# Kernel optimization log

Measured on AMD Instinct MI355X. Metric: run time of the kernel, lower is better.

The kernel has to match this reference:

```python
import jax, jax.numpy as jnp
import numpy as np

N = 50000   # num entities
R2 = 480    # num_rels * 2
D = 200     # h_dim
T = 4       # sequence_len (graph snapshots)
E = 100000  # edges per snapshot
L = 2       # rgcn layers
SLOPE = (1.0 / 8.0 + 1.0 / 3.0) / 2.0  # deterministic rrelu (eval-mode expected slope)


def setup_inputs() -> dict:
    key = jax.random.key(0)
    ks = jax.random.split(key, 13)
    s = 1.0 / np.sqrt(D)
    w = lambda k, shp, sc: jax.random.normal(k, shp, dtype=jnp.float32) * sc
    return {
        "src": jax.random.randint(ks[0], (T, E), 0, N, dtype=jnp.int32),
        "dst": jax.random.randint(ks[1], (T, E), 0, N, dtype=jnp.int32),
        "etype": jax.random.randint(ks[2], (T, E), 0, R2, dtype=jnp.int32),
        "dynamic_emb": w(ks[3], (N, D), 1.0),
        "emb_rel": w(ks[4], (R2, D), s),
        "W_ih": w(ks[5], (3 * D, 2 * D), s),
        "W_hh": w(ks[6], (3 * D, D), s),
        "b_ih": jnp.zeros((3 * D,), jnp.float32),
        "b_hh": jnp.zeros((3 * D,), jnp.float32),
        "W_neighbor": w(ks[7], (L, D, D), s),
        "W_loop": w(ks[8], (L, D, D), s),
        "time_gate_weight": w(ks[9], (D, D), s),
        "time_gate_bias": jnp.zeros((D,), jnp.float32),
    }


def _l2norm(x):
    n = jnp.linalg.norm(x, axis=-1, keepdims=True)
    return x / jnp.maximum(n, 1e-12)


def _gru(x, hprev, W_ih, W_hh, b_ih, b_hh):
    gi = x @ W_ih.T + b_ih
    gh = hprev @ W_hh.T + b_hh
    ir, iz, inn = jnp.split(gi, 3, axis=-1)
    hr, hz, hn = jnp.split(gh, 3, axis=-1)
    r = jax.nn.sigmoid(ir + hr)
    z = jax.nn.sigmoid(iz + hz)
    n = jnp.tanh(inn + r * hn)
    return (1.0 - z) * n + z * hprev


def reference(src, dst, etype, dynamic_emb, emb_rel, W_ih, W_hh, b_ih, b_hh,
              W_neighbor, W_loop, time_gate_weight, time_gate_bias):
    h_init = _l2norm(dynamic_emb)  # layer_norm=True path (F.normalize)

    def step(carry, g):
        h, h0 = carry
        s, d_, et = g
        # per-relation mean of entity embeddings touching that relation (r_to_e spans)
        ent_idx = jnp.concatenate([s, d_])          # [2E]
        seg = jnp.concatenate([et, et])             # [2E]
        ssum = jax.ops.segment_sum(h[ent_idx], seg, num_segments=R2)
        cnt = jax.ops.segment_sum(jnp.ones_like(seg, jnp.float32), seg, num_segments=R2)
        x_mean = ssum / jnp.maximum(cnt, 1.0)[:, None]          # absent rels stay 0
        x_input = jnp.concatenate([emb_rel, x_mean], axis=1)    # [R2, 2D]
        h0 = _l2norm(_gru(x_input, h0, W_ih, W_hh, b_ih, b_hh))
        # UnionRGCNLayer x L: gather -> sum-aggregate -> norm + self-loop -> rrelu
        deg = jax.ops.segment_sum(jnp.ones_like(d_, jnp.float32), d_, num_segments=N)
        norm = 1.0 / jnp.maximum(deg, 1.0)
        hh = h
        for l in range(L):
            pre = hh[s] + h0[et]                                  # [E, D]
            agg = jax.ops.segment_sum(pre, d_, num_segments=N) @ W_neighbor[l]
            out = agg * norm[:, None] + hh @ W_loop[l]
            hh = jnp.where(out >= 0, out, out * SLOPE)            # rrelu (eval)
        cur = _l2norm(hh)
        tw = jax.nn.sigmoid(h @ time_gate_weight + time_gate_bias)
        h = tw * cur + (1.0 - tw) * h
        return (h, h0), h

    (_, _), hist = jax.lax.scan(step, (h_init, emb_rel), (src, dst, etype))
    return hist  # [T, N, D] history of evolved entity embeddings
```

## Files before the change

### kernel.cpp

```cpp
#include <hip/hip_runtime.h>
#include <math.h>

#define NE 50000
#define R2C 480
#define DD 200
#define TT 4
#define EE 100000
#define SLOPE 0.22916666666666666f

#define SCCH 8
#define EPB (256 * SCCH)
#define APAD 224
#define WPAD 224
#define WSZ (208 * WPAD)
#define DCH 4096
#define DNC ((NE + DCH - 1) / DCH)

typedef short short8 __attribute__((ext_vector_type(8)));
typedef float float4v __attribute__((ext_vector_type(4)));

__device__ __forceinline__ float sigm(float x) { return 1.f / (1.f + expf(-x)); }

__device__ __forceinline__ short f2bf(float f) {
  union { float f; unsigned u; } v;
  v.f = f;
  unsigned r = v.u + 0x7fffu + ((v.u >> 16) & 1u);
  return (short)(r >> 16);
}


__global__ void init_h_kernel(const float* __restrict__ emb, float* __restrict__ h) {
  int n = blockIdx.x;
  int lane = threadIdx.x;
  size_t base = (size_t)n * DD;
  float v0 = emb[base + lane];
  float v1 = emb[base + 64 + lane];
  float v2 = emb[base + 128 + lane];
  float v3 = (lane < 8) ? emb[base + 192 + lane] : 0.f;
  float ss = v0 * v0 + v1 * v1 + v2 * v2 + v3 * v3;
#pragma unroll
  for (int off = 32; off; off >>= 1) ss += __shfl_down(ss, off);
  ss = __shfl(ss, 0);
  float inv = 1.f / fmaxf(sqrtf(ss), 1e-12f);
  h[base + lane] = v0 * inv;
  h[base + 64 + lane] = v1 * inv;
  h[base + 128 + lane] = v2 * inv;
  if (lane < 8) h[base + 192 + lane] = v3 * inv;
}

__global__ void copy_kernel(const float* __restrict__ a, float* __restrict__ b, int n) {
  int i = blockIdx.x * blockDim.x + threadIdx.x;
  if (i < n) b[i] = a[i];
}

__global__ void fill_x_kernel(const float* __restrict__ emb_rel, float* __restrict__ X) {
  int i = blockIdx.x * blockDim.x + threadIdx.x;
  if (i >= R2C * DD) return;
  int r = i / DD, d = i - r * DD;
  X[(size_t)r * 400 + d] = emb_rel[i];
}

__global__ void prep_w_kernel(const float* __restrict__ Wnb, const float* __restrict__ Wlp,
                              const float* __restrict__ Wtg, short* __restrict__ Wb) {
  int idx = blockIdx.x * 256 + threadIdx.x;
  if (idx >= 5 * WSZ) return;
  int m = idx / WSZ, rem = idx - m * WSZ;
  int n = rem / WPAD, k = rem - n * WPAD;
  const float* s;
  if (m == 0) s = Wnb;
  else if (m == 1) s = Wnb + DD * DD;
  else if (m == 2) s = Wlp;
  else if (m == 3) s = Wlp + DD * DD;
  else s = Wtg;
  float v = (n < DD && k < DD) ? s[(size_t)k * DD + n] : 0.f;
  Wb[idx] = f2bf(v);
}

__global__ __launch_bounds__(256) void hist_kernel(const int* __restrict__ et,
                                                   const int* __restrict__ dst,
                                                   int* __restrict__ et_hist,
                                                   int* __restrict__ deg_hist) {
  __shared__ int lh[R2C];
  int t = blockIdx.y;
  int tid = threadIdx.x;
  int e0 = blockIdx.x * EPB;
  for (int i = tid; i < R2C; i += 256) lh[i] = 0;
  __syncthreads();
#pragma unroll
  for (int c = 0; c < SCCH; c++) {
    int e = e0 + c * 256 + tid;
    if (e < EE) {
      atomicAdd(&lh[et[(size_t)t * EE + e]], 1);
      atomicAdd(&deg_hist[(size_t)t * NE + dst[(size_t)t * EE + e]], 1);
    }
  }
  __syncthreads();
  for (int i = tid; i < R2C; i += 256)
    if (lh[i]) atomicAdd(&et_hist[t * R2C + i], lh[i]);
}

__global__ void scan_rel_kernel(const int* __restrict__ et_hist, int* __restrict__ rowptr) {
  int t = blockIdx.x;
  int tid = threadIdx.x;
  __shared__ int s[512];
  int v = (tid < R2C) ? 2 * et_hist[t * R2C + tid] : 0;
  s[tid] = v;
  __syncthreads();
  for (int off = 1; off < 512; off <<= 1) {
    int x = (tid >= off) ? s[tid - off] : 0;
    __syncthreads();
    s[tid] += x;
    __syncthreads();
  }
  if (tid < R2C) rowptr[t * (R2C + 1) + tid] = s[tid] - v;
  if (tid == 0) rowptr[t * (R2C + 1) + R2C] = 2 * EE;
}

__global__ __launch_bounds__(256) void deg_partial_kernel(const int* __restrict__ deg_hist,
                                                          int* __restrict__ csum) {
  int t = blockIdx.y, c = blockIdx.x, tid = threadIdx.x;
  const int* dh = deg_hist + (size_t)t * NE;
  int base = c * DCH + tid * 16;
  int s = 0;
  if (base < NE) {
    int end = base + 16 > NE ? NE : base + 16;
    for (int i = base; i < end; i++) s += dh[i];
  }
  __shared__ int red[256];
  red[tid] = s;
  __syncthreads();
  for (int off = 128; off; off >>= 1) {
    if (tid < off) red[tid] += red[tid + off];
    __syncthreads();
  }
  if (tid == 0) csum[t * DNC + c] = red[0];
}

__global__ __launch_bounds__(256) void deg_emit_kernel(const int* __restrict__ deg_hist,
                                                       const int* __restrict__ csum,
                                                       int* __restrict__ rowptr,
                                                       float* __restrict__ normv) {
  int t = blockIdx.y, c = blockIdx.x, tid = threadIdx.x;
  const int* dh = deg_hist + (size_t)t * NE;
  __shared__ int scan[256];
  __shared__ int soff;
  int base = c * DCH + tid * 16;
  int s = 0;
  if (base < NE) {
    int end = base + 16 > NE ? NE : base + 16;
    for (int i = base; i < end; i++) s += dh[i];
  }
  scan[tid] = s;
  __syncthreads();
  for (int off = 1; off < 256; off <<= 1) {
    int x = (tid >= off) ? scan[tid - off] : 0;
    __syncthreads();
    scan[tid] += x;
    __syncthreads();
  }
  if (tid == 0) {
    int o = 0;
    for (int j = 0; j < c; j++) o += csum[t * DNC + j];
    soff = o;
  }
  __syncthreads();
  int run = soff + scan[tid] - s;
  if (base < NE) {
    int end = base + 16 > NE ? NE : base + 16;
    for (int i = base; i < end; i++) {
      int v = dh[i];
      rowptr[t * (NE + 1) + i] = run;
      normv[(size_t)t * NE + i] = 1.f / fmaxf((float)v, 1.f);
      run += v;
    }
  }
  if (c == 0 && tid == 0) rowptr[t * (NE + 1) + NE] = EE;
}

__global__ __launch_bounds__(256) void scatter_rel_kernel(const int* __restrict__ src,
                                                          const int* __restrict__ dst,
                                                          const int* __restrict__ et,
                                                          const int* __restrict__ rowptr,
                                                          int* __restrict__ cursor,
                                                          int* __restrict__ sorted_ent) {
  __shared__ int lcnt[R2C];
  __shared__ int lbase[R2C];
  int t = blockIdx.y;
  int tid = threadIdx.x;
  int e0 = blockIdx.x * EPB;
  for (int i = tid; i < R2C; i += 256) lcnt[i] = 0;
  __syncthreads();
  int rels[SCCH];
#pragma unroll
  for (int c = 0; c < SCCH; c++) {
    int e = e0 + c * 256 + tid;
    int r = (e < EE) ? et[(size_t)t * EE + e] : -1;
    rels[c] = r;
    if (r >= 0) atomicAdd(&lcnt[r], 2);
  }
  __syncthreads();
  const int* rp = rowptr + t * (R2C + 1);
  for (int i = tid; i < R2C; i += 256) {
    int c = lcnt[i];
    lbase[i] = rp[i] + (c ? atomicAdd(&cursor[t * R2C + i], c) : 0);
    lcnt[i] = 0;
  }
  __syncthreads();
  int* se = sorted_ent + (size_t)t * 2 * EE;
#pragma unroll
  for (int c = 0; c < SCCH; c++) {
    int r = rels[c];
    if (r >= 0) {
      int e = e0 + c * 256 + tid;
      int off = atomicAdd(&lcnt[r], 2);
      int p = lbase[r] + off;
      se[p] = src[(size_t)t * EE + e];
      se[p + 1] = dst[(size_t)t * EE + e];
    }
  }
}

__global__ void scatter_dst_kernel(const int* __restrict__ dst, const int* __restrict__ rowptr,
                                   int* __restrict__ cursor, int* __restrict__ sorted_edge) {
  int i = blockIdx.x * blockDim.x + threadIdx.x;
  if (i >= TT * EE) return;
  int t = i / EE, e = i - t * EE;
  int d = dst[i];
  int base = rowptr[t * (NE + 1) + d];
  int p = base + atomicAdd(&cursor[(size_t)t * NE + d], 1);
  sorted_edge[(size_t)t * EE + p] = e;
}


__global__ void relmean_part_kernel(const float* __restrict__ h, const int* __restrict__ rowptr,
                                    const int* __restrict__ sorted_ent_t,
                                    float* __restrict__ Xpart) {
  int r = blockIdx.x, j = blockIdx.y;
  int beg = rowptr[r], end = rowptr[r + 1];
  int lane = threadIdx.x & 63, w = threadIdx.x >> 6;
  float a0 = 0, a1 = 0, a2 = 0, a3 = 0;
  for (int i = beg + j * 4 + w; i < end; i += 16) {
    int idx = sorted_ent_t[i];
    const float* row = h + (size_t)idx * DD;
    a0 += row[lane];
    a1 += row[64 + lane];
    a2 += row[128 + lane];
    if (lane < 8) a3 += row[192 + lane];
  }
  __shared__ float part[4][DD];
  part[w][lane] = a0;
  part[w][64 + lane] = a1;
  part[w][128 + lane] = a2;
  if (lane < 8) part[w][192 + lane] = a3;
  __syncthreads();
  for (int d = threadIdx.x; d < DD; d += 256) {
    Xpart[((size_t)r * 4 + j) * DD + d] = part[0][d] + part[1][d] + part[2][d] + part[3][d];
  }
}

__global__ void relmean_comb_kernel(const float* __restrict__ Xpart,
                                    const int* __restrict__ rowptr, float* __restrict__ X) {
  int r = blockIdx.x;
  int d = threadIdx.x;
  if (d >= DD) return;
  float s = 0.f;
#pragma unroll
  for (int j = 0; j < 4; j++) s += Xpart[((size_t)r * 4 + j) * DD + d];
  float cnt = fmaxf((float)(rowptr[r + 1] - rowptr[r]), 1.f);
  X[(size_t)r * 400 + 200 + d] = s / cnt;
}

__global__ __launch_bounds__(256) void gemm_small_bt(const float* __restrict__ A,
                                                     const float* __restrict__ B,
                                                     float* __restrict__ C, int M, int N, int K) {
  __shared__ float As[16][33];
  __shared__ float Bs[16][33];
  int tid = threadIdx.x;
  int col0 = blockIdx.x * 32;
  int row0 = blockIdx.y * 32;
  int tr = tid >> 4, tc = tid & 15;
  float a00 = 0, a01 = 0, a10 = 0, a11 = 0;
  for (int k0 = 0; k0 < K; k0 += 16) {
    __syncthreads();
    for (int i = tid; i < 512; i += 256) {
      int kk = i & 15, r = i >> 4;
      int row = row0 + r, k = k0 + kk;
      As[kk][r] = (row < M && k < K) ? A[(size_t)row * K + k] : 0.f;
    }
    for (int i = tid; i < 512; i += 256) {
      int kk = i & 15, c = i >> 4;
      int col = col0 + c, k = k0 + kk;
      Bs[kk][c] = (col < N && k < K) ? B[(size_t)col * K + k] : 0.f;
    }
    __syncthreads();
#pragma unroll
    for (int kk = 0; kk < 16; kk++) {
      float x0 = As[kk][tr * 2], x1 = As[kk][tr * 2 + 1];
      float y0 = Bs[kk][tc * 2], y1 = Bs[kk][tc * 2 + 1];
      a00 += x0 * y0;
      a01 += x0 * y1;
      a10 += x1 * y0;
      a11 += x1 * y1;
    }
  }
  int row = row0 + tr * 2, col = col0 + tc * 2;
  if (row < M && col < N) C[(size_t)row * N + col] = a00;
  if (row < M && col + 1 < N) C[(size_t)row * N + col + 1] = a01;
  if (row + 1 < M && col < N) C[(size_t)(row + 1) * N + col] = a10;
  if (row + 1 < M && col + 1 < N) C[(size_t)(row + 1) * N + col + 1] = a11;
}

__global__ void gru_gate_kernel(const float* __restrict__ gi, const float* __restrict__ gh,
                                const float* __restrict__ b_ih, const float* __restrict__ b_hh,
                                float* __restrict__ h0) {
  int r = blockIdx.x;
  int tid = threadIdx.x;
  int lane = tid & 63, w = tid >> 6;
  __shared__ float red[4];
  float o = 0.f;
  if (tid < DD) {
    size_t b = (size_t)r * (3 * DD);
    float ir = gi[b + tid] + b_ih[tid];
    float iz = gi[b + DD + tid] + b_ih[DD + tid];
    float inn = gi[b + 2 * DD + tid] + b_ih[2 * DD + tid];
    float hr = gh[b + tid] + b_hh[tid];
    float hz = gh[b + DD + tid] + b_hh[DD + tid];
    float hn = gh[b + 2 * DD + tid] + b_hh[2 * DD + tid];
    float hv = h0[(size_t)r * DD + tid];
    float rr = sigm(ir + hr);
    float z = sigm(iz + hz);
    float n = tanhf(inn + rr * hn);
    o = (1.f - z) * n + z * hv;
  }
  float ss = o * o;
#pragma unroll
  for (int off = 32; off; off >>= 1) ss += __shfl_down(ss, off);
  if (lane == 0) red[w] = ss;
  __syncthreads();
  float tot = red[0] + red[1] + red[2] + red[3];
  float inv = 1.f / fmaxf(sqrtf(tot), 1e-12f);
  if (tid < DD) h0[(size_t)r * DD + tid] = o * inv;
}

__global__ void agg_kernel(const float* __restrict__ hh, const float* __restrict__ h0,
                           const int* __restrict__ rowptr, const int* __restrict__ sorted_edge_t,
                           const int* __restrict__ src_t, const int* __restrict__ et_t,
                           const float* __restrict__ normv_t, short* __restrict__ aggb) {
  int w = threadIdx.x >> 6, lane = threadIdx.x & 63;
  int n = blockIdx.x * 4 + w;
  if (n >= NE) return;
  int beg = rowptr[n], end = rowptr[n + 1];
  float a0 = 0, a1 = 0, a2 = 0, a3 = 0;
  for (int i = beg; i < end; i++) {
    int e = sorted_edge_t[i];
    const float* hr = hh + (size_t)src_t[e] * DD;
    const float* qr = h0 + (size_t)et_t[e] * DD;
    a0 += hr[lane] + qr[lane];
    a1 += hr[64 + lane] + qr[64 + lane];
    a2 += hr[128 + lane] + qr[128 + lane];
    if (lane < 8) a3 += hr[192 + lane] + qr[192 + lane];
  }
  float nm = normv_t[n];
  short* outp = aggb + (size_t)n * APAD;
  outp[lane] = f2bf(a0 * nm);
  outp[64 + lane] = f2bf(a1 * nm);
  outp[128 + lane] = f2bf(a2 * nm);
  if (lane < 8) outp[192 + lane] = f2bf(a3 * nm);
  else if (lane < 32) outp[192 + lane] = 0;
}


__global__ __launch_bounds__(256) void gemm_dual(const short* __restrict__ A1,
                                                 const short* __restrict__ Wb1,
                                                 const float* __restrict__ A2,
                                                 const short* __restrict__ Wb2,
                                                 float* __restrict__ C) {
  __shared__ short Bt[2][208][40];
  int tid = threadIdx.x;
  int lane = tid & 63, w = tid >> 6;
  int quad = lane >> 4, l16 = lane & 15;
  int row = blockIdx.x * 64 + w * 16 + l16;
  bool rok = row < NE;

  short8 af1[7], af2[7];
#pragma unroll
  for (int c = 0; c < 7; c++) {
    af1[c] = rok ? *(const short8*)(A1 + (size_t)row * APAD + c * 32 + quad * 8)
                 : (short8){0, 0, 0, 0, 0, 0, 0, 0};
  }
#pragma unroll
  for (int c = 0; c < 7; c++) {
    int kb = c * 32 + quad * 8;
    short8 a = (short8){0, 0, 0, 0, 0, 0, 0, 0};
    if (rok && kb < DD) {
      const float* ap = A2 + (size_t)row * DD + kb;
      float4v v0 = *(const float4v*)ap;
      float4v v1 = *(const float4v*)(ap + 4);
      short tmp[8] = {f2bf(v0[0]), f2bf(v0[1]), f2bf(v0[2]), f2bf(v0[3]),
                      f2bf(v1[0]), f2bf(v1[1]), f2bf(v1[2]), f2bf(v1[3])};
      a = *(short8*)&tmp[0];
    }
    af2[c] = a;
  }

  float4v acc[13];
#pragma unroll
  for (int ct = 0; ct < 13; ct++) acc[ct] = (float4v){0.f, 0.f, 0.f, 0.f};

#pragma unroll
  for (int c = 0; c < 7; c++) {
    __syncthreads();
#pragma unroll
    for (int it = 0; it < 7; it++) {
      int s = tid + it * 256;
      if (s < 1664) {
        int m = s >= 832;
        int ss = s - m * 832;
        int n = ss % 208, k8 = (ss / 208) * 8;
        const short* Wb = m ? Wb2 : Wb1;
        *(short8*)&Bt[m][n][k8] = *(const short8*)&Wb[(size_t)n * WPAD + c * 32 + k8];
      }
    }
    __syncthreads();
#pragma unroll
    for (int ct = 0; ct < 13; ct++) {
      short8 b1 = *(short8*)&Bt[0][ct * 16 + l16][quad * 8];
      short8 b2 = *(short8*)&Bt[1][ct * 16 + l16][quad * 8];
      acc[ct] = __builtin_amdgcn_mfma_f32_16x16x32_bf16(af1[c], b1, acc[ct], 0, 0, 0);
      acc[ct] = __builtin_amdgcn_mfma_f32_16x16x32_bf16(af2[c], b2, acc[ct], 0, 0, 0);
    }
  }
  int r0 = blockIdx.x * 64 + w * 16 + quad * 4;
#pragma unroll
  for (int ct = 0; ct < 13; ct++) {
    int col = ct * 16 + l16;
    if (col >= DD) continue;
#pragma unroll
    for (int i = 0; i < 4; i++) {
      int r = r0 + i;
      if (r < NE) {
        float v = acc[ct][i];
        v = (v >= 0.f) ? v : v * SLOPE;
        C[(size_t)r * DD + col] = v;
      }
    }
  }
}

__global__ __launch_bounds__(256) void gemm_tgfin(const float* __restrict__ A,
                                                  const short* __restrict__ Wb,
                                                  const float* __restrict__ hh,
                                                  const float* __restrict__ tgb,
                                                  float* __restrict__ outp) {
  __shared__ short Bt[208][40];
  int tid = threadIdx.x;
  int lane = tid & 63, w = tid >> 6;
  int quad = lane >> 4, l16 = lane & 15;
  int row = blockIdx.x * 64 + w * 16 + l16;
  bool rok = row < NE;

  short8 af[7];
#pragma unroll
  for (int c = 0; c < 7; c++) {
    int kb = c * 32 + quad * 8;
    short8 a = (short8){0, 0, 0, 0, 0, 0, 0, 0};
    if (rok && kb < DD) {
      const float* ap = A + (size_t)row * DD + kb;
      float4v v0 = *(const float4v*)ap;
      float4v v1 = *(const float4v*)(ap + 4);
      short tmp[8] = {f2bf(v0[0]), f2bf(v0[1]), f2bf(v0[2]), f2bf(v0[3]),
                      f2bf(v1[0]), f2bf(v1[1]), f2bf(v1[2]), f2bf(v1[3])};
      a = *(short8*)&tmp[0];
    }
    af[c] = a;
  }

  float4v acc[13];
#pragma unroll
  for (int ct = 0; ct < 13; ct++) acc[ct] = (float4v){0.f, 0.f, 0.f, 0.f};

#pragma unroll
  for (int c = 0; c < 7; c++) {
    __syncthreads();
#pragma unroll
    for (int it = 0; it < 4; it++) {
      int s = tid + it * 256;
      if (s < 832) {
        int n = s % 208, k8 = (s / 208) * 8;
        *(short8*)&Bt[n][k8] = *(const short8*)&Wb[(size_t)n * WPAD + c * 32 + k8];
      }
    }
    __syncthreads();
#pragma unroll
    for (int ct = 0; ct < 13; ct++) {
      short8 bf = *(short8*)&Bt[ct * 16 + l16][quad * 8];
      acc[ct] = __builtin_amdgcn_mfma_f32_16x16x32_bf16(af[c], bf, acc[ct], 0, 0, 0);
    }
  }
  int rbase = blockIdx.x * 64 + w * 16 + quad * 4;
#pragma unroll
  for (int i = 0; i < 4; i++) {
    int r = rbase + i;
    bool ok = r < NE;
    size_t rb = (size_t)r * DD;
    float ssq = 0.f;
#pragma unroll
    for (int ct = 0; ct < 13; ct++) {
      int col = ct * 16 + l16;
      float x = (ok && col < DD) ? hh[rb + col] : 0.f;
      ssq += x * x;
    }
#pragma unroll
    for (int off = 1; off < 16; off <<= 1) ssq += __shfl_xor(ssq, off);
    float inv = 1.f / fmaxf(sqrtf(ssq), 1e-12f);
#pragma unroll
    for (int ct = 0; ct < 13; ct++) {
      int col = ct * 16 + l16;
      if (ok && col < DD) {
        float cur = hh[rb + col] * inv;
        float tw = sigm(acc[ct][i] + tgb[col]);
        outp[rb + col] = tw * cur + (1.f - tw) * A[rb + col];
      }
    }
  }
}


extern "C" void kernel_launch(void* const* d_in, const int* in_sizes, int n_in, void* d_out,
                              int out_size, void* d_ws, size_t ws_size, hipStream_t stream) {
  const int* src = (const int*)d_in[0];
  const int* dst = (const int*)d_in[1];
  const int* et = (const int*)d_in[2];
  const float* dyn = (const float*)d_in[3];
  const float* emb_rel = (const float*)d_in[4];
  const float* W_ih = (const float*)d_in[5];
  const float* W_hh = (const float*)d_in[6];
  const float* b_ih = (const float*)d_in[7];
  const float* b_hh = (const float*)d_in[8];
  const float* W_nb = (const float*)d_in[9];
  const float* W_lp = (const float*)d_in[10];
  const float* Wtg = (const float*)d_in[11];
  const float* tgb = (const float*)d_in[12];
  float* out = (float*)d_out;

  char* p = (char*)d_ws;
  float* h = (float*)p;        p += (size_t)NE * DD * 4;
  float* bufB = (float*)p;     p += (size_t)NE * DD * 4;
  float* agg = (float*)p;      p += (size_t)NE * DD * 4;
  float* h0 = (float*)p;       p += (size_t)R2C * DD * 4;
  float* X = (float*)p;        p += (size_t)R2C * 400 * 4;
  float* normv = (float*)p;    p += (size_t)TT * NE * 4;
  int* et_rowptr = (int*)p;    p += (size_t)TT * (R2C + 1) * 4;
  int* et_cursor = (int*)p;    p += (size_t)TT * R2C * 4;
  int* et_hist = (int*)p;      p += (size_t)TT * R2C * 4;
  int* sorted_ent = (int*)p;   p += (size_t)TT * 2 * EE * 4;
  int* dst_rowptr = (int*)p;   p += (size_t)TT * (NE + 1) * 4;
  int* dst_cursor = (int*)p;   p += (size_t)TT * NE * 4;
  int* deg_hist = (int*)p;     p += (size_t)TT * NE * 4;
  int* sorted_edge = (int*)p;  p += (size_t)TT * EE * 4;
  short* Wb = (short*)p;       p += (size_t)5 * WSZ * 2;
  float* Xpart = (float*)p;    p += (size_t)R2C * 4 * DD * 4;
  int* csum = (int*)p;         p += (size_t)TT * DNC * 4;

  float* gi = bufB;
  float* gh = bufB + (size_t)R2C * 3 * DD;
  short* aggb = (short*)agg;

  hipMemsetAsync(et_hist, 0, (size_t)TT * R2C * 4, stream);
  hipMemsetAsync(deg_hist, 0, (size_t)TT * NE * 4, stream);
  hipMemsetAsync(et_cursor, 0, (size_t)TT * R2C * 4, stream);
  hipMemsetAsync(dst_cursor, 0, (size_t)TT * NE * 4, stream);

  init_h_kernel<<<NE, 64, 0, stream>>>(dyn, h);
  copy_kernel<<<(R2C * DD + 255) / 256, 256, 0, stream>>>(emb_rel, h0, R2C * DD);
  fill_x_kernel<<<(R2C * DD + 255) / 256, 256, 0, stream>>>(emb_rel, X);
  prep_w_kernel<<<(5 * WSZ + 255) / 256, 256, 0, stream>>>(W_nb, W_lp, Wtg, Wb);
  const dim3 bin_grid((EE + EPB - 1) / EPB, TT);
  hist_kernel<<<bin_grid, 256, 0, stream>>>(et, dst, et_hist, deg_hist);
  scan_rel_kernel<<<TT, 512, 0, stream>>>(et_hist, et_rowptr);
  const dim3 deg_grid(DNC, TT);
  deg_partial_kernel<<<deg_grid, 256, 0, stream>>>(deg_hist, csum);
  deg_emit_kernel<<<deg_grid, 256, 0, stream>>>(deg_hist, csum, dst_rowptr, normv);
  scatter_rel_kernel<<<bin_grid, 256, 0, stream>>>(src, dst, et, et_rowptr, et_cursor, sorted_ent);
  scatter_dst_kernel<<<(TT * EE + 255) / 256, 256, 0, stream>>>(dst, dst_rowptr, dst_cursor,
                                                                sorted_edge);

  const int gemm_grid = (NE + 63) / 64;
  const dim3 gru_grid((3 * DD + 31) / 32, (R2C + 31) / 32);
  const dim3 rm_grid(R2C, 4);
  for (int t = 0; t < TT; t++) {
    const int* src_t = src + (size_t)t * EE;
    const int* et_t = et + (size_t)t * EE;
    const float* hcur = (t == 0) ? h : out + (size_t)(t - 1) * NE * DD;
    float* bufA = out + (size_t)t * NE * DD;

    relmean_part_kernel<<<rm_grid, 256, 0, stream>>>(hcur, et_rowptr + t * (R2C + 1),
                                                     sorted_ent + (size_t)t * 2 * EE, Xpart);
    relmean_comb_kernel<<<R2C, 256, 0, stream>>>(Xpart, et_rowptr + t * (R2C + 1), X);
    gemm_small_bt<<<gru_grid, 256, 0, stream>>>(X, W_ih, gi, R2C, 3 * DD, 2 * DD);
    gemm_small_bt<<<gru_grid, 256, 0, stream>>>(h0, W_hh, gh, R2C, 3 * DD, DD);
    gru_gate_kernel<<<R2C, 256, 0, stream>>>(gi, gh, b_ih, b_hh, h0);
    agg_kernel<<<(NE + 3) / 4, 256, 0, stream>>>(hcur, h0, dst_rowptr + t * (NE + 1),
                                                 sorted_edge + (size_t)t * EE, src_t, et_t,
                                                 normv + (size_t)t * NE, aggb);
    gemm_dual<<<gemm_grid, 256, 0, stream>>>(aggb, Wb + 0 * WSZ, hcur, Wb + 2 * WSZ, bufA);
    agg_kernel<<<(NE + 3) / 4, 256, 0, stream>>>(bufA, h0, dst_rowptr + t * (NE + 1),
                                                 sorted_edge + (size_t)t * EE, src_t, et_t,
                                                 normv + (size_t)t * NE, aggb);
    gemm_dual<<<gemm_grid, 256, 0, stream>>>(aggb, Wb + 1 * WSZ, bufA, Wb + 3 * WSZ, bufB);
    gemm_tgfin<<<gemm_grid, 256, 0, stream>>>(hcur, Wb + 4 * WSZ, bufB, tgb, bufA);
  }
}
```

Before: 1.568 ms.

## Make GEMM kernels persistent with whole weight matrix resident in LDS

```diff
diff --git a/kernel.cpp b/kernel.cpp
--- a/kernel.cpp
+++ b/kernel.cpp
@@ -15,6 +15,7 @@
 #define WSZ (208 * WPAD)
 #define DCH 4096
 #define DNC ((NE + DCH - 1) / DCH)
+#define NTILE 3125
 
 typedef short short8 __attribute__((ext_vector_type(8)));
 typedef float float4v __attribute__((ext_vector_type(4)));
@@ -370,153 +371,124 @@
 }
 
 
-__global__ __launch_bounds__(256) void gemm_dual(const short* __restrict__ A1,
-                                                 const short* __restrict__ Wb1,
-                                                 const float* __restrict__ A2,
-                                                 const short* __restrict__ Wb2,
-                                                 float* __restrict__ C) {
-  __shared__ short Bt[2][208][40];
-  int tid = threadIdx.x;
+__device__ __forceinline__ short8 ldA_f32(const float* __restrict__ ap) {
+  float4v v0 = *(const float4v*)ap;
+  float4v v1 = *(const float4v*)(ap + 4);
+  short tmp[8] = {f2bf(v0[0]), f2bf(v0[1]), f2bf(v0[2]), f2bf(v0[3]),
+                  f2bf(v1[0]), f2bf(v1[1]), f2bf(v1[2]), f2bf(v1[3])};
+  return *(short8*)&tmp[0];
+}
+
+__global__ __launch_bounds__(512, 2) void gemm_dual(const short* __restrict__ A1,
+                                                    const short* __restrict__ Wb1,
+                                                    const float* __restrict__ A2,
+                                                    const short* __restrict__ Wb2,
+                                                    float* __restrict__ C) {
+  __shared__ __align__(16) short Bt[2][200][200];
+  int tid = threadIdx.x;
+  for (int s = tid; s < 10000; s += 512) {
+    int m = s >= 5000;
+    int ss = s - m * 5000;
+    int n = ss / 25, k8 = (ss - n * 25) * 8;
+    const short* W = m ? Wb2 : Wb1;
+    *(short8*)&Bt[m][n][k8] = *(const short8*)&W[(size_t)n * WPAD + k8];
+  }
+  __syncthreads();
   int lane = tid & 63, w = tid >> 6;
   int quad = lane >> 4, l16 = lane & 15;
-  int row = blockIdx.x * 64 + w * 16 + l16;
-  bool rok = row < NE;
-
-  short8 af1[7], af2[7];
-#pragma unroll
-  for (int c = 0; c < 7; c++) {
-    af1[c] = rok ? *(const short8*)(A1 + (size_t)row * APAD + c * 32 + quad * 8)
-                 : (short8){0, 0, 0, 0, 0, 0, 0, 0};
-  }
-#pragma unroll
-  for (int c = 0; c < 7; c++) {
-    int kb = c * 32 + quad * 8;
-    short8 a = (short8){0, 0, 0, 0, 0, 0, 0, 0};
-    if (rok && kb < DD) {
-      const float* ap = A2 + (size_t)row * DD + kb;
-      float4v v0 = *(const float4v*)ap;
-      float4v v1 = *(const float4v*)(ap + 4);
-      short tmp[8] = {f2bf(v0[0]), f2bf(v0[1]), f2bf(v0[2]), f2bf(v0[3]),
-                      f2bf(v1[0]), f2bf(v1[1]), f2bf(v1[2]), f2bf(v1[3])};
-      a = *(short8*)&tmp[0];
-    }
-    af2[c] = a;
-  }
-
-  float4v acc[13];
-#pragma unroll
-  for (int ct = 0; ct < 13; ct++) acc[ct] = (float4v){0.f, 0.f, 0.f, 0.f};
-
-#pragma unroll
-  for (int c = 0; c < 7; c++) {
-    __syncthreads();
-#pragma unroll
-    for (int it = 0; it < 7; it++) {
-      int s = tid + it * 256;
-      if (s < 1664) {
-        int m = s >= 832;
-        int ss = s - m * 832;
-        int n = ss % 208, k8 = (ss / 208) * 8;
-        const short* Wb = m ? Wb2 : Wb1;
-        *(short8*)&Bt[m][n][k8] = *(const short8*)&Wb[(size_t)n * WPAD + c * 32 + k8];
+  for (int ti = w * 256 + blockIdx.x; ti < NTILE; ti += 2048) {
+    int arow = ti * 16 + l16;
+    short8 af1[7], af2[7];
+#pragma unroll
+    for (int c = 0; c < 7; c++)
+      af1[c] = *(const short8*)(A1 + (size_t)arow * APAD + c * 32 + quad * 8);
+#pragma unroll
+    for (int c = 0; c < 7; c++) {
+      int kb = c * 32 + quad * 8;
+      af2[c] = (kb < DD) ? ldA_f32(A2 + (size_t)arow * DD + kb) : (short8){0, 0, 0, 0, 0, 0, 0, 0};
+    }
+    float4v acc[13];
+#pragma unroll
+    for (int ct = 0; ct < 13; ct++) acc[ct] = (float4v){0.f, 0.f, 0.f, 0.f};
+#pragma unroll
+    for (int c = 0; c < 7; c++) {
+      int kb = (c == 6 && quad > 0) ? quad * 8 : c * 32 + quad * 8;
+#pragma unroll
+      for (int ct = 0; ct < 13; ct++) {
+        int col = (ct < 12 ? ct * 16 : 184) + l16;
+        short8 b1 = *(const short8*)&Bt[0][col][kb];
+        short8 b2 = *(const short8*)&Bt[1][col][kb];
+        acc[ct] = __builtin_amdgcn_mfma_f32_16x16x32_bf16(af1[c], b1, acc[ct], 0, 0, 0);
+        acc[ct] = __builtin_amdgcn_mfma_f32_16x16x32_bf16(af2[c], b2, acc[ct], 0, 0, 0);
       }
     }
-    __syncthreads();
+    int r0 = ti * 16 + quad * 4;
 #pragma unroll
     for (int ct = 0; ct < 13; ct++) {
-      short8 b1 = *(short8*)&Bt[0][ct * 16 + l16][quad * 8];
-      short8 b2 = *(short8*)&Bt[1][ct * 16 + l16][quad * 8];
-      acc[ct] = __builtin_amdgcn_mfma_f32_16x16x32_bf16(af1[c], b1, acc[ct], 0, 0, 0);
-      acc[ct] = __builtin_amdgcn_mfma_f32_16x16x32_bf16(af2[c], b2, acc[ct], 0, 0, 0);
-    }
-  }
-  int r0 = blockIdx.x * 64 + w * 16 + quad * 4;
-#pragma unroll
-  for (int ct = 0; ct < 13; ct++) {
-    int col = ct * 16 + l16;
-    if (col >= DD) continue;
-#pragma unroll
-    for (int i = 0; i < 4; i++) {
-      int r = r0 + i;
-      if (r < NE) {
+      int col = (ct < 12 ? ct * 16 : 184) + l16;
+#pragma unroll
+      for (int i = 0; i < 4; i++) {
         float v = acc[ct][i];
         v = (v >= 0.f) ? v : v * SLOPE;
-        C[(size_t)r * DD + col] = v;
+        C[(size_t)(r0 + i) * DD + col] = v;
       }
     }
   }
 }
 
-__global__ __launch_bounds__(256) void gemm_tgfin(const float* __restrict__ A,
-                                                  const short* __restrict__ Wb,
-                                                  const float* __restrict__ hh,
-                                                  const float* __restrict__ tgb,
-                                                  float* __restrict__ outp) {
-  __shared__ short Bt[208][40];
-  int tid = threadIdx.x;
+__global__ __launch_bounds__(512, 4) void gemm_tgfin(const float* __restrict__ A,
+                                                     const short* __restrict__ Wb,
+                                                     const float* __restrict__ hh,
+                                                     const float* __restrict__ tgb,
+                                                     float* __restrict__ outp) {
+  __shared__ __align__(16) short Bt[200][200];
+  int tid = threadIdx.x;
+  for (int s = tid; s < 5000; s += 512) {
+    int n = s / 25, k8 = (s - n * 25) * 8;
+    *(short8*)&Bt[n][k8] = *(const short8*)&Wb[(size_t)n * WPAD + k8];
+  }
+  __syncthreads();
   int lane = tid & 63, w = tid >> 6;
   int quad = lane >> 4, l16 = lane & 15;
-  int row = blockIdx.x * 64 + w * 16 + l16;
-  bool rok = row < NE;
-
-  short8 af[7];
-#pragma unroll
-  for (int c = 0; c < 7; c++) {
-    int kb = c * 32 + quad * 8;
-    short8 a = (short8){0, 0, 0, 0, 0, 0, 0, 0};
-    if (rok && kb < DD) {
-      const float* ap = A + (size_t)row * DD + kb;
-      float4v v0 = *(const float4v*)ap;
-      float4v v1 = *(const float4v*)(ap + 4);
-      short tmp[8] = {f2bf(v0[0]), f2bf(v0[1]), f2bf(v0[2]), f2bf(v0[3]),
-                      f2bf(v1[0]), f2bf(v1[1]), f2bf(v1[2]), f2bf(v1[3])};
-      a = *(short8*)&tmp[0];
-    }
-    af[c] = a;
-  }
-
-  float4v acc[13];
-#pragma unroll
-  for (int ct = 0; ct < 13; ct++) acc[ct] = (float4v){0.f, 0.f, 0.f, 0.f};
-
-#pragma unroll
-  for (int c = 0; c < 7; c++) {
-    __syncthreads();
-#pragma unroll
-    for (int it = 0; it < 4; it++) {
-      int s = tid + it * 256;
-      if (s < 832) {
-        int n = s % 208, k8 = (s / 208) * 8;
-        *(short8*)&Bt[n][k8] = *(const short8*)&Wb[(size_t)n * WPAD + c * 32 + k8];
+  for (int ti = w * 256 + blockIdx.x; ti < NTILE; ti += 2048) {
+    int arow = ti * 16 + l16;
+    short8 af[7];
+#pragma unroll
+    for (int c = 0; c < 7; c++) {
+      int kb = c * 32 + quad * 8;
+      af[c] = (kb < DD) ? ldA_f32(A + (size_t)arow * DD + kb) : (short8){0, 0, 0, 0, 0, 0, 0, 0};
+    }
+    float4v acc[13];
+#pragma unroll
+    for (int ct = 0; ct < 13; ct++) acc[ct] = (float4v){0.f, 0.f, 0.f, 0.f};
+#pragma unroll
+    for (int c = 0; c < 7; c++) {
+      int kb = (c == 6 && quad > 0) ? quad * 8 : c * 32 + quad * 8;
+#pragma unroll
+      for (int ct = 0; ct < 13; ct++) {
+        int col = (ct < 12 ? ct * 16 : 184) + l16;
+        short8 b = *(const short8*)&Bt[col][kb];
+        acc[ct] = __builtin_amdgcn_mfma_f32_16x16x32_bf16(af[c], b, acc[ct], 0, 0, 0);
       }
     }
-    __syncthreads();
-#pragma unroll
-    for (int ct = 0; ct < 13; ct++) {
-      short8 bf = *(short8*)&Bt[ct * 16 + l16][quad * 8];
-      acc[ct] = __builtin_amdgcn_mfma_f32_16x16x32_bf16(af[c], bf, acc[ct], 0, 0, 0);
-    }
-  }
-  int rbase = blockIdx.x * 64 + w * 16 + quad * 4;
-#pragma unroll
-  for (int i = 0; i < 4; i++) {
-    int r = rbase + i;
-    bool ok = r < NE;
-    size_t rb = (size_t)r * DD;
-    float ssq = 0.f;
-#pragma unroll
-    for (int ct = 0; ct < 13; ct++) {
-      int col = ct * 16 + l16;
-      float x = (ok && col < DD) ? hh[rb + col] : 0.f;
-      ssq += x * x;
-    }
-#pragma unroll
-    for (int off = 1; off < 16; off <<= 1) ssq += __shfl_xor(ssq, off);
-    float inv = 1.f / fmaxf(sqrtf(ssq), 1e-12f);
-#pragma unroll
-    for (int ct = 0; ct < 13; ct++) {
-      int col = ct * 16 + l16;
-      if (ok && col < DD) {
+    int rbase = ti * 16 + quad * 4;
+#pragma unroll
+    for (int i = 0; i < 4; i++) {
+      int r = rbase + i;
+      size_t rb = (size_t)r * DD;
+      float ssq = 0.f;
+#pragma unroll
+      for (int ct = 0; ct < 13; ct++) {
+        int col = (ct < 12 ? ct * 16 : 184) + l16;
+        float x = (ct == 12 && l16 < 8) ? 0.f : hh[rb + col];
+        ssq += x * x;
+      }
+#pragma unroll
+      for (int off = 1; off < 16; off <<= 1) ssq += __shfl_xor(ssq, off);
+      float inv = 1.f / fmaxf(sqrtf(ssq), 1e-12f);
+#pragma unroll
+      for (int ct = 0; ct < 13; ct++) {
+        int col = (ct < 12 ? ct * 16 : 184) + l16;
         float cur = hh[rb + col] * inv;
         float tw = sigm(acc[ct][i] + tgb[col]);
         outp[rb + col] = tw * cur + (1.f - tw) * A[rb + col];
@@ -585,7 +557,6 @@
   scatter_dst_kernel<<<(TT * EE + 255) / 256, 256, 0, stream>>>(dst, dst_rowptr, dst_cursor,
                                                                 sorted_edge);
 
-  const int gemm_grid = (NE + 63) / 64;
   const dim3 gru_grid((3 * DD + 31) / 32, (R2C + 31) / 32);
   const dim3 rm_grid(R2C, 4);
   for (int t = 0; t < TT; t++) {
@@ -603,11 +574,11 @@
     agg_kernel<<<(NE + 3) / 4, 256, 0, stream>>>(hcur, h0, dst_rowptr + t * (NE + 1),
                                                  sorted_edge + (size_t)t * EE, src_t, et_t,
                                                  normv + (size_t)t * NE, aggb);
-    gemm_dual<<<gemm_grid, 256, 0, stream>>>(aggb, Wb + 0 * WSZ, hcur, Wb + 2 * WSZ, bufA);
+    gemm_dual<<<256, 512, 0, stream>>>(aggb, Wb + 0 * WSZ, hcur, Wb + 2 * WSZ, bufA);
     agg_kernel<<<(NE + 3) / 4, 256, 0, stream>>>(bufA, h0, dst_rowptr + t * (NE + 1),
                                                  sorted_edge + (size_t)t * EE, src_t, et_t,
                                                  normv + (size_t)t * NE, aggb);
-    gemm_dual<<<gemm_grid, 256, 0, stream>>>(aggb, Wb + 1 * WSZ, bufA, Wb + 3 * WSZ, bufB);
-    gemm_tgfin<<<gemm_grid, 256, 0, stream>>>(hcur, Wb + 4 * WSZ, bufB, tgb, bufA);
-  }
-}
+    gemm_dual<<<256, 512, 0, stream>>>(aggb, Wb + 1 * WSZ, bufA, Wb + 3 * WSZ, bufB);
+    gemm_tgfin<<<256, 512, 0, stream>>>(hcur, Wb + 4 * WSZ, bufB, tgb, bufA);
+  }
+}
```

Result: slower. 3.785 ms (+141.3%).
